# Performance work log

Measured on AMD Instinct MI355X. Metric: run time of the kernel, lower is better.

Reference implementation:

```python
import jax, jax.numpy as jnp
import numpy as np

N = 400000
H = 256          # hidden_dim
NUM_HEADS = 4
HEAD_DIM = H // NUM_HEADS
B = 1024         # number of graphs (segments)


def setup_inputs() -> dict:
    key = jax.random.key(0)
    ks = jax.random.split(key, 6)
    x = jax.random.normal(ks[0], (N, H), dtype=jnp.float32)
    batch = jnp.sort(jax.random.randint(ks[1], (N,), 0, B, dtype=jnp.int64))
    s = 1.0 / np.sqrt(H)
    W1 = jax.random.normal(ks[2], (H, H), dtype=jnp.float32) * s
    b1 = jnp.zeros((H,), dtype=jnp.float32)
    W2 = jax.random.normal(ks[3], (H, NUM_HEADS), dtype=jnp.float32) * s
    b2 = jnp.zeros((NUM_HEADS,), dtype=jnp.float32)
    Wt = jax.random.normal(ks[4], (H, H), dtype=jnp.float32) * s
    bt = jnp.zeros((H,), dtype=jnp.float32)
    return {"x": x, "batch": batch, "W1": W1, "b1": b1, "W2": W2, "b2": b2, "Wt": Wt, "bt": bt}


def reference(x, batch, W1, b1, W2, b2, Wt, bt):
    # attention MLP: Linear -> Tanh -> Linear  -> [N, num_heads]
    logits = jnp.tanh(x @ W1 + b1) @ W2 + b2
    # segment (per-graph) softmax over nodes, per head (PyG-style with 1e-16 eps)
    seg_max = jax.ops.segment_max(logits, batch, num_segments=B)        # [B, heads]
    e = jnp.exp(logits - seg_max[batch])                                # [N, heads]
    seg_sum = jax.ops.segment_sum(e, batch, num_segments=B)             # [B, heads]
    attn = e / (seg_sum[batch] + 1e-16)                                 # [N, heads]
    # transform + per-head weighting
    xt = (x @ Wt + bt).reshape(N, NUM_HEADS, HEAD_DIM)
    weighted = (attn[:, :, None] * xt).reshape(N, H)
    # global add pool over each graph
    graph_emb = jax.ops.segment_sum(weighted, batch, num_segments=B)    # [B, hidden]
    return graph_emb, attn
```

## Files before the change

kernel.cpp:

```cpp
#include <hip/hip_runtime.h>
#include <math.h>

#define HD    256
#define NHEAD 4
#define NSEG  1024
#define RPB   64
#define NRB64 6250

typedef short bf16x8 __attribute__((ext_vector_type(8)));
typedef float f32x16 __attribute__((ext_vector_type(16)));

__device__ __forceinline__ float tanh_fast(float v) {
    float e = __expf(2.0f * v);
    return 1.0f - 2.0f * __builtin_amdgcn_rcpf(e + 1.0f);
}

__device__ __forceinline__ void split2(float a, float b, unsigned &hi, unsigned &lo) {
    unsigned ba = __float_as_uint(a), bb = __float_as_uint(b);
    unsigned ha = ba & 0xFFFF0000u, hb = bb & 0xFFFF0000u;
    float la = a - __uint_as_float(ha);
    float lb = b - __uint_as_float(hb);
    hi = (ha >> 16) | hb;
    lo = (__float_as_uint(la) >> 16) | (__float_as_uint(lb) & 0xFFFF0000u);
}

__device__ __forceinline__ void gld16(const void* g, void* l) {
    __builtin_amdgcn_global_load_lds(
        (const __attribute__((address_space(1))) void*)g,
        (__attribute__((address_space(3))) void*)l, 16, 0, 0);
}

__global__ __launch_bounds__(256) void k0_prep(
    const float* __restrict__ W1, char* __restrict__ ws)
{
    int g = blockIdx.x * 256 + threadIdx.x;
    int c  = g & 127;
    int j  = (g >> 7) & 3;
    int o  = (g >> 9) & 1;
    int ch = (g >> 10) & 1;
    int t  = g >> 11;
    int k   = t*16 + o*8 + 2*j;
    int col = ch*128 + c;
    float a = W1[(size_t)k * HD + col];
    float b = W1[(size_t)(k + 1) * HD + col];
    unsigned hw, lw;
    split2(a, b, hw, lw);
    size_t off = (size_t)t*16384 + ch*8192 + o*2048 + c*16 + j*4;
    *(unsigned*)(ws + off)        = hw;
    *(unsigned*)(ws + off + 4096) = lw;
}

#define K1_THREADS 256
#define BUFB 12288
#define K1_LDS 33792

__global__ __launch_bounds__(K1_THREADS, 4) void k1_mfma(
    const float* __restrict__ x, const char* __restrict__ wsW,
    const float* __restrict__ b1, const float* __restrict__ W2,
    const float* __restrict__ b2, float* __restrict__ lgA,
    float* __restrict__ lgB, int N)
{
    extern __shared__ __align__(16) char smem[];

    const int raw = blockIdx.x;
    const int ch  = (raw >> 3) & 1;
    const int rb  = (raw >> 4) * 8 + (raw & 7);
    if (rb >= NRB64) return;

    const int tid  = threadIdx.x;
    const int lane = tid & 63;
    const int lo5  = lane & 31;
    const int hi   = lane >> 5;
    const int wid  = tid >> 6;
    const int rg   = wid >> 1;
    const int cg   = wid & 1;
    const int blkrow = rb * RPB;
    const int rl   = rg*32 + lo5;

    f32x16 acc[2];
    #pragma unroll
    for (int ct = 0; ct < 2; ++ct) {
        float b1v = b1[ch*128 + cg*64 + ct*32 + lo5];
        #pragma unroll
        for (int e = 0; e < 16; ++e) acc[ct][e] = b1v;
    }

    const char* gwbase = wsW + ch*8192 + tid*16;
    const char* gxbase;
    {
        int row  = tid >> 2;
        int slot = tid & 3;
        long grow = blkrow + row; if (grow > N-1) grow = N-1;
        gxbase = (const char*)x + grow*1024 + ((slot ^ (row & 3)) * 16);
    }

    auto STAGE = [&](int u) {
        const int db = (u & 1) * BUFB;
        const char* w = gwbase + (size_t)u*16384;
        #pragma unroll
        for (int i = 0; i < 2; ++i)
            gld16(w + i*4096, smem + db + i*4096 + tid*16);
        gld16(gxbase + (size_t)u*64, smem + db + 8192 + tid*16);
    };

    STAGE(0);
    __syncthreads();

    #pragma unroll
    for (int t = 0; t < 16; ++t) {
        if (t < 15) STAGE(t + 1);
        const int buf = (t & 1) * BUFB;
        {
            union { unsigned u[4]; bf16x8 v; } ah, al;
            {
                const int s0 = hi*2;
                const int xb = buf + 8192 + rl*64;
                float4 q0 = *(const float4*)(smem + xb + ((s0     ^ (rl & 3)) << 4));
                float4 q1 = *(const float4*)(smem + xb + (((s0+1) ^ (rl & 3)) << 4));
                split2(q0.x, q0.y, ah.u[0], al.u[0]);
                split2(q0.z, q0.w, ah.u[1], al.u[1]);
                split2(q1.x, q1.y, ah.u[2], al.u[2]);
                split2(q1.z, q1.w, ah.u[3], al.u[3]);
            }
            bf16x8 bh[2], bl[2];
            #pragma unroll
            for (int ct = 0; ct < 2; ++ct) {
                int off = buf + hi*2048 + (cg*64 + ct*32 + lo5)*16;
                bh[ct] = *(const bf16x8*)(smem + off);
                bl[ct] = *(const bf16x8*)(smem + off + 4096);
            }
            #pragma unroll
            for (int ct = 0; ct < 2; ++ct) {
                acc[ct] = __builtin_amdgcn_mfma_f32_32x32x16_bf16(ah.v, bh[ct], acc[ct], 0, 0, 0);
                acc[ct] = __builtin_amdgcn_mfma_f32_32x32x16_bf16(ah.v, bl[ct], acc[ct], 0, 0, 0);
                acc[ct] = __builtin_amdgcn_mfma_f32_32x32x16_bf16(al.v, bh[ct], acc[ct], 0, 0, 0);
            }
        }
        __syncthreads();
    }

    #pragma unroll
    for (int ct = 0; ct < 2; ++ct) {
        const int col = cg*64 + ct*32 + lo5;
        #pragma unroll
        for (int e = 0; e < 16; ++e) {
            float h = tanh_fast(acc[ct][e]);
            int row = rg*32 + (e & 3) + 8*(e >> 2) + 4*hi;
            unsigned hh = __float_as_uint(h) & 0xFFFF0000u;
            float hl = h - __uint_as_float(hh);
            int byte = row*256 + ((((col >> 3) ^ (row & 15))) << 4) + (col & 7)*2;
            *(unsigned short*)(smem + byte)         = (unsigned short)(hh >> 16);
            *(unsigned short*)(smem + 16384 + byte) = (unsigned short)(__float_as_uint(hl) >> 16);
        }
    }
    __syncthreads();

    float* p_lds = (float*)(smem + 32768);
    if (wid < 2) {
        const int rt  = wid;
        const int row = rt*32 + lo5;
        const int colh = lo5 & 3;
        const bool act = lo5 < 4;
        f32x16 d;
        #pragma unroll
        for (int e = 0; e < 16; ++e) d[e] = 0.0f;
        #pragma unroll
        for (int kk = 0; kk < 8; ++kk) {
            int sb = row*256 + (((kk*2 + hi) ^ (row & 15)) << 4);
            bf16x8 ahh = *(const bf16x8*)(smem + sb);
            bf16x8 alo = *(const bf16x8*)(smem + 16384 + sb);
            union { unsigned short s[8]; bf16x8 v; } wh, wl;
            #pragma unroll
            for (int j = 0; j < 8; ++j) {
                float w = W2[(size_t)(ch*128 + kk*16 + hi*8 + j)*NHEAD + colh];
                w = act ? w : 0.0f;
                unsigned hb = __float_as_uint(w) & 0xFFFF0000u;
                float wlf = w - __uint_as_float(hb);
                wh.s[j] = (unsigned short)(hb >> 16);
                wl.s[j] = (unsigned short)(__float_as_uint(wlf) >> 16);
            }
            d = __builtin_amdgcn_mfma_f32_32x32x16_bf16(ahh, wh.v, d, 0, 0, 0);
            d = __builtin_amdgcn_mfma_f32_32x32x16_bf16(ahh, wl.v, d, 0, 0, 0);
            d = __builtin_amdgcn_mfma_f32_32x32x16_bf16(alo, wh.v, d, 0, 0, 0);
        }
        if (act) {
            #pragma unroll
            for (int e = 0; e < 16; ++e) {
                int r = rt*32 + (e & 3) + 8*(e >> 2) + 4*hi;
                p_lds[r*4 + lo5] = d[e];
            }
        }
    }
    __syncthreads();
    if (tid < RPB) {
        int grow = blkrow + tid;
        if (grow < N) {
            float4 o = *(float4*)(p_lds + tid*4);
            float* dst;
            if (ch == 0) {
                o.x += b2[0]; o.y += b2[1]; o.z += b2[2]; o.w += b2[3];
                dst = lgA;
            } else dst = lgB;
            *(float4*)(dst + (size_t)grow * NHEAD) = o;
        }
    }
}

__device__ __forceinline__ int lower_bound(const int* __restrict__ a, int n, int v) {
    int lo = 0, hi = n;
    while (lo < hi) { int m = (lo + hi) >> 1; if (a[m] < v) lo = m + 1; else hi = m; }
    return lo;
}

__global__ __launch_bounds__(256) void k2_seg(
    const int* __restrict__ batch, const float* __restrict__ lgA,
    const float* __restrict__ lgB, float* __restrict__ out, int N)
{
    const int b = blockIdx.x;
    const int tid = threadIdx.x;
    const int lane = tid & 63, wid = tid >> 6;
    const int start = lower_bound(batch, N, b);
    const int end   = lower_bound(batch, N, b + 1);
    const float4* la4 = (const float4*)lgA;
    const float4* lb4 = (const float4*)lgB;

    float4 mx = make_float4(-INFINITY, -INFINITY, -INFINITY, -INFINITY);
    for (int i = start + tid; i < end; i += 256) {
        float4 a = la4[i], bq = lb4[i];
        mx.x = fmaxf(mx.x, a.x + bq.x); mx.y = fmaxf(mx.y, a.y + bq.y);
        mx.z = fmaxf(mx.z, a.z + bq.z); mx.w = fmaxf(mx.w, a.w + bq.w);
    }
    #pragma unroll
    for (int ofs = 32; ofs >= 1; ofs >>= 1) {
        mx.x = fmaxf(mx.x, __shfl_xor(mx.x, ofs, 64));
        mx.y = fmaxf(mx.y, __shfl_xor(mx.y, ofs, 64));
        mx.z = fmaxf(mx.z, __shfl_xor(mx.z, ofs, 64));
        mx.w = fmaxf(mx.w, __shfl_xor(mx.w, ofs, 64));
    }
    __shared__ float4 red[4];
    if (lane == 0) red[wid] = mx;
    __syncthreads();
    float4 smax;
    smax.x = fmaxf(fmaxf(red[0].x, red[1].x), fmaxf(red[2].x, red[3].x));
    smax.y = fmaxf(fmaxf(red[0].y, red[1].y), fmaxf(red[2].y, red[3].y));
    smax.z = fmaxf(fmaxf(red[0].z, red[1].z), fmaxf(red[2].z, red[3].z));
    smax.w = fmaxf(fmaxf(red[0].w, red[1].w), fmaxf(red[2].w, red[3].w));
    __syncthreads();

    float4 sm = make_float4(0.f, 0.f, 0.f, 0.f);
    for (int i = start + tid; i < end; i += 256) {
        float4 a = la4[i], bq = lb4[i];
        sm.x += __expf(a.x + bq.x - smax.x); sm.y += __expf(a.y + bq.y - smax.y);
        sm.z += __expf(a.z + bq.z - smax.z); sm.w += __expf(a.w + bq.w - smax.w);
    }
    #pragma unroll
    for (int ofs = 32; ofs >= 1; ofs >>= 1) {
        sm.x += __shfl_xor(sm.x, ofs, 64);
        sm.y += __shfl_xor(sm.y, ofs, 64);
        sm.z += __shfl_xor(sm.z, ofs, 64);
        sm.w += __shfl_xor(sm.w, ofs, 64);
    }
    if (lane == 0) red[wid] = sm;
    __syncthreads();
    if (tid == 0) {
        float4 ssum;
        ssum.x = red[0].x + red[1].x + red[2].x + red[3].x;
        ssum.y = red[0].y + red[1].y + red[2].y + red[3].y;
        ssum.z = red[0].z + red[1].z + red[2].z + red[3].z;
        ssum.w = red[0].w + red[1].w + red[2].w + red[3].w;
        *(float4*)(out + (size_t)b * HD)     = smax;
        *(float4*)(out + (size_t)b * HD + 4) = ssum;
    }
}

__global__ __launch_bounds__(256) void k3_pool(
    const int* __restrict__ batch, const float* __restrict__ x,
    const float* __restrict__ Wt, const float* __restrict__ bt,
    const float* __restrict__ lgB, float* __restrict__ out, int N)
{
    const int b = blockIdx.x;
    const int tid = threadIdx.x;
    const int start = lower_bound(batch, N, b);
    const int end   = lower_bound(batch, N, b + 1);

    float4* at4 = (float4*)(out + (size_t)NSEG * HD);
    const float4* lb4 = (const float4*)lgB;

    const float4 smax = *(const float4*)(out + (size_t)b * HD);
    const float4 ssum = *(const float4*)(out + (size_t)b * HD + 4);
    float4 inv;
    inv.x = 1.0f / (ssum.x + 1e-16f); inv.y = 1.0f / (ssum.y + 1e-16f);
    inv.z = 1.0f / (ssum.z + 1e-16f); inv.w = 1.0f / (ssum.w + 1e-16f);

    float z0 = 0.f, z1 = 0.f, z2 = 0.f, z3 = 0.f;
    __shared__ float4 attn_s[256];

    for (int c0 = start; c0 < end; c0 += 256) {
        const int idx = c0 + tid;
        if (idx < end) {
            float4 l = at4[idx];
            float4 lb = lb4[idx];
            float4 a;
            a.x = __expf(l.x + lb.x - smax.x) * inv.x;
            a.y = __expf(l.y + lb.y - smax.y) * inv.y;
            a.z = __expf(l.z + lb.z - smax.z) * inv.z;
            a.w = __expf(l.w + lb.w - smax.w) * inv.w;
            at4[idx] = a;
            attn_s[tid] = a;
        }
        __syncthreads();
        const int cnt = min(256, end - c0);
        const float* xb = x + (size_t)c0 * HD + tid;
        #pragma unroll 4
        for (int i = 0; i < cnt; ++i) {
            float4 a = attn_s[i];
            float xv = xb[(size_t)i * HD];
            z0 = fmaf(a.x, xv, z0); z1 = fmaf(a.y, xv, z1);
            z2 = fmaf(a.z, xv, z2); z3 = fmaf(a.w, xv, z3);
        }
        __syncthreads();
    }

    __shared__ float zs[NHEAD][HD];
    zs[0][tid] = z0; zs[1][tid] = z1; zs[2][tid] = z2; zs[3][tid] = z3;
    __syncthreads();

    const int h = tid >> 6;
    float smh, invh;
    if      (h == 0) { smh = ssum.x; invh = inv.x; }
    else if (h == 1) { smh = ssum.y; invh = inv.y; }
    else if (h == 2) { smh = ssum.z; invh = inv.z; }
    else             { smh = ssum.w; invh = inv.w; }

    float acc = smh * invh * bt[tid];
    #pragma unroll 4
    for (int k = 0; k < HD; ++k)
        acc = fmaf(zs[h][k], Wt[(size_t)k * HD + tid], acc);

    out[(size_t)b * HD + tid] = acc;
}

extern "C" void kernel_launch(void* const* d_in, const int* in_sizes, int n_in,
                              void* d_out, int out_size, void* d_ws, size_t ws_size,
                              hipStream_t stream) {
    const float* x   = (const float*)d_in[0];
    const int*   bat = (const int*)  d_in[1];
    const float* W1  = (const float*)d_in[2];
    const float* b1  = (const float*)d_in[3];
    const float* W2  = (const float*)d_in[4];
    const float* b2  = (const float*)d_in[5];
    const float* Wt  = (const float*)d_in[6];
    const float* bt  = (const float*)d_in[7];
    float* out = (float*)d_out;
    const int N = in_sizes[0] / HD;

    float* lgA = out + (size_t)NSEG * HD;
    char*  wsW = (char*)d_ws;
    float* lgB = (float*)((char*)d_ws + 262144);

    hipLaunchKernelGGL(k0_prep, dim3(128), dim3(256), 0, stream, W1, wsW);
    hipLaunchKernelGGL(k1_mfma, dim3(((NRB64 + 7) / 8) * 16), dim3(K1_THREADS),
                       K1_LDS, stream, x, wsW, b1, W2, b2, lgA, lgB, N);
    hipLaunchKernelGGL(k2_seg, dim3(NSEG), dim3(256), 0, stream, bat, lgA, lgB, out, N);
    hipLaunchKernelGGL(k3_pool, dim3(NSEG), dim3(256), 0, stream, bat, x, Wt, bt, lgB, out, N);
}
```

Before: 372.9 us.

## Compute full hidden width per block and drop x low-part MFMA

```diff
diff --git a/kernel.cpp b/kernel.cpp
--- a/kernel.cpp
+++ b/kernel.cpp
@@ -4,8 +4,8 @@
 #define HD    256
 #define NHEAD 4
 #define NSEG  1024
-#define RPB   64
-#define NRB64 6250
+#define RPB   128
+#define NRB   3125
 
 typedef short bf16x8 __attribute__((ext_vector_type(8)));
 typedef float f32x16 __attribute__((ext_vector_type(16)));
@@ -22,6 +22,12 @@
     float lb = b - __uint_as_float(hb);
     hi = (ha >> 16) | hb;
     lo = (__float_as_uint(la) >> 16) | (__float_as_uint(lb) & 0xFFFF0000u);
+}
+
+__device__ __forceinline__ unsigned cvt_pk_bf16(float a, float b) {
+    unsigned r;
+    asm("v_cvt_pk_bf16_f32 %0, %1, %2" : "=v"(r) : "v"(a), "v"(b));
+    return r;
 }
 
 __device__ __forceinline__ void gld16(const void* g, void* l) {
@@ -50,42 +56,38 @@
     *(unsigned*)(ws + off + 4096) = lw;
 }
 
-#define K1_THREADS 256
-#define BUFB 12288
-#define K1_LDS 33792
+#define K1_THREADS 512
+#define BUFB 24576
+#define K1_LDS 49152
 
 __global__ __launch_bounds__(K1_THREADS, 4) void k1_mfma(
     const float* __restrict__ x, const char* __restrict__ wsW,
     const float* __restrict__ b1, const float* __restrict__ W2,
-    const float* __restrict__ b2, float* __restrict__ lgA,
-    float* __restrict__ lgB, int N)
+    const float* __restrict__ b2, float* __restrict__ lg, int N)
 {
     extern __shared__ __align__(16) char smem[];
 
-    const int raw = blockIdx.x;
-    const int ch  = (raw >> 3) & 1;
-    const int rb  = (raw >> 4) * 8 + (raw & 7);
-    if (rb >= NRB64) return;
-
+    const int rb = blockIdx.x;
     const int tid  = threadIdx.x;
     const int lane = tid & 63;
     const int lo5  = lane & 31;
     const int hi   = lane >> 5;
     const int wid  = tid >> 6;
-    const int rg   = wid >> 1;
-    const int cg   = wid & 1;
+    const int rg   = wid >> 2;
+    const int cgi  = wid & 3;
     const int blkrow = rb * RPB;
-    const int rl   = rg*32 + lo5;
-
-    f32x16 acc[2];
+
+    f32x16 acc[2][2];
     #pragma unroll
     for (int ct = 0; ct < 2; ++ct) {
-        float b1v = b1[ch*128 + cg*64 + ct*32 + lo5];
+        float b1v = b1[cgi*64 + ct*32 + lo5];
         #pragma unroll
-        for (int e = 0; e < 16; ++e) acc[ct][e] = b1v;
-    }
-
-    const char* gwbase = wsW + ch*8192 + tid*16;
+        for (int rt = 0; rt < 2; ++rt)
+            #pragma unroll
+            for (int e = 0; e < 16; ++e) acc[rt][ct][e] = b1v;
+    }
+
+    const char* gwbase = wsW + tid*16;
     const char* gxbase;
     {
         int row  = tid >> 2;
@@ -96,11 +98,10 @@
 
     auto STAGE = [&](int u) {
         const int db = (u & 1) * BUFB;
+        gld16(gxbase + (size_t)u*64, smem + db + tid*16);
         const char* w = gwbase + (size_t)u*16384;
-        #pragma unroll
-        for (int i = 0; i < 2; ++i)
-            gld16(w + i*4096, smem + db + i*4096 + tid*16);
-        gld16(gxbase + (size_t)u*64, smem + db + 8192 + tid*16);
+        gld16(w,        smem + db + 8192  + tid*16);
+        gld16(w + 8192, smem + db + 16384 + tid*16);
     };
 
     STAGE(0);
@@ -110,99 +111,102 @@
     for (int t = 0; t < 16; ++t) {
         if (t < 15) STAGE(t + 1);
         const int buf = (t & 1) * BUFB;
-        {
-            union { unsigned u[4]; bf16x8 v; } ah, al;
-            {
-                const int s0 = hi*2;
-                const int xb = buf + 8192 + rl*64;
-                float4 q0 = *(const float4*)(smem + xb + ((s0     ^ (rl & 3)) << 4));
-                float4 q1 = *(const float4*)(smem + xb + (((s0+1) ^ (rl & 3)) << 4));
-                split2(q0.x, q0.y, ah.u[0], al.u[0]);
-                split2(q0.z, q0.w, ah.u[1], al.u[1]);
-                split2(q1.x, q1.y, ah.u[2], al.u[2]);
-                split2(q1.z, q1.w, ah.u[3], al.u[3]);
-            }
-            bf16x8 bh[2], bl[2];
+        union { unsigned u[4]; bf16x8 v; } ah[2];
+        #pragma unroll
+        for (int rt = 0; rt < 2; ++rt) {
+            const int rl = rg*64 + rt*32 + lo5;
+            const int xb = buf + rl*64;
+            const int s0 = hi*2;
+            float4 q0 = *(const float4*)(smem + xb + ((s0     ^ (rl & 3)) << 4));
+            float4 q1 = *(const float4*)(smem + xb + (((s0+1) ^ (rl & 3)) << 4));
+            ah[rt].u[0] = cvt_pk_bf16(q0.x, q0.y);
+            ah[rt].u[1] = cvt_pk_bf16(q0.z, q0.w);
+            ah[rt].u[2] = cvt_pk_bf16(q1.x, q1.y);
+            ah[rt].u[3] = cvt_pk_bf16(q1.z, q1.w);
+        }
+        bf16x8 bh[2], bl[2];
+        #pragma unroll
+        for (int ct = 0; ct < 2; ++ct) {
+            const int col = cgi*64 + ct*32 + lo5;
+            const int off = buf + 8192 + (col >> 7)*8192 + hi*2048 + (col & 127)*16;
+            bh[ct] = *(const bf16x8*)(smem + off);
+            bl[ct] = *(const bf16x8*)(smem + off + 4096);
+        }
+        #pragma unroll
+        for (int rt = 0; rt < 2; ++rt)
             #pragma unroll
             for (int ct = 0; ct < 2; ++ct) {
-                int off = buf + hi*2048 + (cg*64 + ct*32 + lo5)*16;
-                bh[ct] = *(const bf16x8*)(smem + off);
-                bl[ct] = *(const bf16x8*)(smem + off + 4096);
-            }
+                acc[rt][ct] = __builtin_amdgcn_mfma_f32_32x32x16_bf16(ah[rt].v, bh[ct], acc[rt][ct], 0, 0, 0);
+                acc[rt][ct] = __builtin_amdgcn_mfma_f32_32x32x16_bf16(ah[rt].v, bl[ct], acc[rt][ct], 0, 0, 0);
+            }
+        __syncthreads();
+    }
+
+    float* p_lds = (float*)(smem + 32768);
+    #pragma unroll
+    for (int p = 0; p < 4; ++p) {
+        if (rg == (p >> 1)) {
+            const int rt = p & 1;
             #pragma unroll
             for (int ct = 0; ct < 2; ++ct) {
-                acc[ct] = __builtin_amdgcn_mfma_f32_32x32x16_bf16(ah.v, bh[ct], acc[ct], 0, 0, 0);
-                acc[ct] = __builtin_amdgcn_mfma_f32_32x32x16_bf16(ah.v, bl[ct], acc[ct], 0, 0, 0);
-                acc[ct] = __builtin_amdgcn_mfma_f32_32x32x16_bf16(al.v, bh[ct], acc[ct], 0, 0, 0);
-            }
-        }
-        __syncthreads();
-    }
-
-    #pragma unroll
-    for (int ct = 0; ct < 2; ++ct) {
-        const int col = cg*64 + ct*32 + lo5;
-        #pragma unroll
-        for (int e = 0; e < 16; ++e) {
-            float h = tanh_fast(acc[ct][e]);
-            int row = rg*32 + (e & 3) + 8*(e >> 2) + 4*hi;
-            unsigned hh = __float_as_uint(h) & 0xFFFF0000u;
-            float hl = h - __uint_as_float(hh);
-            int byte = row*256 + ((((col >> 3) ^ (row & 15))) << 4) + (col & 7)*2;
-            *(unsigned short*)(smem + byte)         = (unsigned short)(hh >> 16);
-            *(unsigned short*)(smem + 16384 + byte) = (unsigned short)(__float_as_uint(hl) >> 16);
-        }
-    }
-    __syncthreads();
-
-    float* p_lds = (float*)(smem + 32768);
-    if (wid < 2) {
-        const int rt  = wid;
-        const int row = rt*32 + lo5;
-        const int colh = lo5 & 3;
-        const bool act = lo5 < 4;
-        f32x16 d;
-        #pragma unroll
-        for (int e = 0; e < 16; ++e) d[e] = 0.0f;
-        #pragma unroll
-        for (int kk = 0; kk < 8; ++kk) {
-            int sb = row*256 + (((kk*2 + hi) ^ (row & 15)) << 4);
-            bf16x8 ahh = *(const bf16x8*)(smem + sb);
-            bf16x8 alo = *(const bf16x8*)(smem + 16384 + sb);
-            union { unsigned short s[8]; bf16x8 v; } wh, wl;
-            #pragma unroll
-            for (int j = 0; j < 8; ++j) {
-                float w = W2[(size_t)(ch*128 + kk*16 + hi*8 + j)*NHEAD + colh];
-                w = act ? w : 0.0f;
-                unsigned hb = __float_as_uint(w) & 0xFFFF0000u;
-                float wlf = w - __uint_as_float(hb);
-                wh.s[j] = (unsigned short)(hb >> 16);
-                wl.s[j] = (unsigned short)(__float_as_uint(wlf) >> 16);
-            }
-            d = __builtin_amdgcn_mfma_f32_32x32x16_bf16(ahh, wh.v, d, 0, 0, 0);
-            d = __builtin_amdgcn_mfma_f32_32x32x16_bf16(ahh, wl.v, d, 0, 0, 0);
-            d = __builtin_amdgcn_mfma_f32_32x32x16_bf16(alo, wh.v, d, 0, 0, 0);
-        }
-        if (act) {
-            #pragma unroll
-            for (int e = 0; e < 16; ++e) {
-                int r = rt*32 + (e & 3) + 8*(e >> 2) + 4*hi;
-                p_lds[r*4 + lo5] = d[e];
-            }
-        }
-    }
-    __syncthreads();
-    if (tid < RPB) {
-        int grow = blkrow + tid;
-        if (grow < N) {
-            float4 o = *(float4*)(p_lds + tid*4);
-            float* dst;
-            if (ch == 0) {
+                const int col = cgi*64 + ct*32 + lo5;
+                #pragma unroll
+                for (int e = 0; e < 16; ++e) {
+                    float h = tanh_fast(acc[rt][ct][e]);
+                    int row = (e & 3) + 8*(e >> 2) + 4*hi;
+                    unsigned hh = __float_as_uint(h) & 0xFFFF0000u;
+                    float hl = h - __uint_as_float(hh);
+                    int byte = row*512 + (((col >> 3) ^ row) << 4) + (col & 7)*2;
+                    *(unsigned short*)(smem + byte)         = (unsigned short)(hh >> 16);
+                    *(unsigned short*)(smem + 16384 + byte) = (unsigned short)(__float_as_uint(hl) >> 16);
+                }
+            }
+        }
+        __syncthreads();
+        if (wid == 0) {
+            const int row  = lo5;
+            const int colh = lo5 & 3;
+            const bool act = lo5 < 4;
+            f32x16 d;
+            #pragma unroll
+            for (int e = 0; e < 16; ++e) d[e] = 0.0f;
+            #pragma unroll
+            for (int kk = 0; kk < 16; ++kk) {
+                int sb = row*512 + (((kk*2 + hi) ^ row) << 4);
+                bf16x8 ahh = *(const bf16x8*)(smem + sb);
+                bf16x8 alo = *(const bf16x8*)(smem + 16384 + sb);
+                union { unsigned short s[8]; bf16x8 v; } wh, wl;
+                #pragma unroll
+                for (int j = 0; j < 8; ++j) {
+                    float w = W2[(size_t)(kk*16 + hi*8 + j)*NHEAD + colh];
+                    w = act ? w : 0.0f;
+                    unsigned hb = __float_as_uint(w) & 0xFFFF0000u;
+                    float wlf = w - __uint_as_float(hb);
+                    wh.s[j] = (unsigned short)(hb >> 16);
+                    wl.s[j] = (unsigned short)(__float_as_uint(wlf) >> 16);
+                }
+                d = __builtin_amdgcn_mfma_f32_32x32x16_bf16(ahh, wh.v, d, 0, 0, 0);
+                d = __builtin_amdgcn_mfma_f32_32x32x16_bf16(ahh, wl.v, d, 0, 0, 0);
+                d = __builtin_amdgcn_mfma_f32_32x32x16_bf16(alo, wh.v, d, 0, 0, 0);
+            }
+            if (act) {
+                #pragma unroll
+                for (int e = 0; e < 16; ++e) {
+                    int r = (e & 3) + 8*(e >> 2) + 4*hi;
+                    p_lds[r*4 + lo5] = d[e];
+                }
+            }
+        }
+        __syncthreads();
+        if (tid < 32) {
+            int grow = blkrow + p*32 + tid;
+            if (grow < N) {
+                float4 o = *(float4*)(p_lds + tid*4);
                 o.x += b2[0]; o.y += b2[1]; o.z += b2[2]; o.w += b2[3];
-                dst = lgA;
-            } else dst = lgB;
-            *(float4*)(dst + (size_t)grow * NHEAD) = o;
-        }
+                *(float4*)(lg + (size_t)grow * NHEAD) = o;
+            }
+        }
+        __syncthreads();
     }
 }
 
@@ -213,22 +217,21 @@
 }
 
 __global__ __launch_bounds__(256) void k2_seg(
-    const int* __restrict__ batch, const float* __restrict__ lgA,
-    const float* __restrict__ lgB, float* __restrict__ out, int N)
+    const int* __restrict__ batch, const float* __restrict__ lg,
+    float* __restrict__ out, int N)
 {
     const int b = blockIdx.x;
     const int tid = threadIdx.x;
     const int lane = tid & 63, wid = tid >> 6;
     const int start = lower_bound(batch, N, b);
     const int end   = lower_bound(batch, N, b + 1);
-    const float4* la4 = (const float4*)lgA;
-    const float4* lb4 = (const float4*)lgB;
+    const float4* lg4 = (const float4*)lg;
 
     float4 mx = make_float4(-INFINITY, -INFINITY, -INFINITY, -INFINITY);
     for (int i = start + tid; i < end; i += 256) {
-        float4 a = la4[i], bq = lb4[i];
-        mx.x = fmaxf(mx.x, a.x + bq.x); mx.y = fmaxf(mx.y, a.y + bq.y);
-        mx.z = fmaxf(mx.z, a.z + bq.z); mx.w = fmaxf(mx.w, a.w + bq.w);
+        float4 l = lg4[i];
+        mx.x = fmaxf(mx.x, l.x); mx.y = fmaxf(mx.y, l.y);
+        mx.z = fmaxf(mx.z, l.z); mx.w = fmaxf(mx.w, l.w);
     }
     #pragma unroll
     for (int ofs = 32; ofs >= 1; ofs >>= 1) {
@@ -249,9 +252,9 @@
 
     float4 sm = make_float4(0.f, 0.f, 0.f, 0.f);
     for (int i = start + tid; i < end; i += 256) {
-        float4 a = la4[i], bq = lb4[i];
-        sm.x += __expf(a.x + bq.x - smax.x); sm.y += __expf(a.y + bq.y - smax.y);
-        sm.z += __expf(a.z + bq.z - smax.z); sm.w += __expf(a.w + bq.w - smax.w);
+        float4 l = lg4[i];
+        sm.x += __expf(l.x - smax.x); sm.y += __expf(l.y - smax.y);
+        sm.z += __expf(l.z - smax.z); sm.w += __expf(l.w - smax.w);
     }
     #pragma unroll
     for (int ofs = 32; ofs >= 1; ofs >>= 1) {
@@ -276,7 +279,7 @@
 __global__ __launch_bounds__(256) void k3_pool(
     const int* __restrict__ batch, const float* __restrict__ x,
     const float* __restrict__ Wt, const float* __restrict__ bt,
-    const float* __restrict__ lgB, float* __restrict__ out, int N)
+    float* __restrict__ out, int N)
 {
     const int b = blockIdx.x;
     const int tid = threadIdx.x;
@@ -284,7 +287,6 @@
     const int end   = lower_bound(batch, N, b + 1);
 
     float4* at4 = (float4*)(out + (size_t)NSEG * HD);
-    const float4* lb4 = (const float4*)lgB;
 
     const float4 smax = *(const float4*)(out + (size_t)b * HD);
     const float4 ssum = *(const float4*)(out + (size_t)b * HD + 4);
@@ -299,12 +301,11 @@
         const int idx = c0 + tid;
         if (idx < end) {
             float4 l = at4[idx];
-            float4 lb = lb4[idx];
             float4 a;
-            a.x = __expf(l.x + lb.x - smax.x) * inv.x;
-            a.y = __expf(l.y + lb.y - smax.y) * inv.y;
-            a.z = __expf(l.z + lb.z - smax.z) * inv.z;
-            a.w = __expf(l.w + lb.w - smax.w) * inv.w;
+            a.x = __expf(l.x - smax.x) * inv.x;
+            a.y = __expf(l.y - smax.y) * inv.y;
+            a.z = __expf(l.z - smax.z) * inv.z;
+            a.w = __expf(l.w - smax.w) * inv.w;
             at4[idx] = a;
             attn_s[tid] = a;
         }
@@ -354,13 +355,12 @@
     float* out = (float*)d_out;
     const int N = in_sizes[0] / HD;
 
-    float* lgA = out + (size_t)NSEG * HD;
+    float* lg  = out + (size_t)NSEG * HD;
     char*  wsW = (char*)d_ws;
-    float* lgB = (float*)((char*)d_ws + 262144);
 
     hipLaunchKernelGGL(k0_prep, dim3(128), dim3(256), 0, stream, W1, wsW);
-    hipLaunchKernelGGL(k1_mfma, dim3(((NRB64 + 7) / 8) * 16), dim3(K1_THREADS),
-                       K1_LDS, stream, x, wsW, b1, W2, b2, lgA, lgB, N);
-    hipLaunchKernelGGL(k2_seg, dim3(NSEG), dim3(256), 0, stream, bat, lgA, lgB, out, N);
-    hipLaunchKernelGGL(k3_pool, dim3(NSEG), dim3(256), 0, stream, bat, x, Wt, bt, lgB, out, N);
-}
+    hipLaunchKernelGGL(k1_mfma, dim3(NRB), dim3(K1_THREADS),
+                       K1_LDS, stream, x, wsW, b1, W2, b2, lg, N);
+    hipLaunchKernelGGL(k2_seg, dim3(NSEG), dim3(256), 0, stream, bat, lg, out, N);
+    hipLaunchKernelGGL(k3_pool, dim3(NSEG), dim3(256), 0, stream, bat, x, Wt, bt, out, N);
+}
```

Result: slower. 408.4 us (+9.5%).
